# Performance work log

Hardware: AMD Instinct MI355X
Metric: run time of the kernel (lower is better)

## Reference

```python
import jax, jax.numpy as jnp
import numpy as np

B = 1; C = 96; NH = 4; HD = 24; WIN = 3; LL = 27; SR = 8
Dd, Hh, Ww = 16, 40, 40
N = Dd * Hh * Ww
pH, pW, pD = Hh // SR, Ww // SR, Dd // SR
PL = pH * pW * pD
T = 4096


def _build_mask():
    p = WIN // 2
    m = np.zeros((Dd + 2 * p, Hh + 2 * p, Ww + 2 * p), bool)
    m[p:Dd + p, p:Hh + p, p:Ww + p] = True
    pats = np.stack([m[dz:dz + Dd, dy:dy + Hh, dx:dx + Ww]
                     for dz in range(WIN) for dy in range(WIN) for dx in range(WIN)], axis=-1)
    return jnp.asarray(~pats.reshape(N, LL))  # True where padded (masked)

MASK = _build_mask()


def _layernorm(x, w, b, eps=1e-5):
    mu = jnp.mean(x, axis=-1, keepdims=True)
    var = jnp.var(x, axis=-1, keepdims=True)
    return (x - mu) / jnp.sqrt(var + eps) * w + b


def _l2(x, eps=1e-12):
    n = jnp.sqrt(jnp.sum(x * x, axis=-1, keepdims=True))
    return x / jnp.maximum(n, eps)


def _unfold3d(x):
    # x: (B,C,D,H,W) -> (B,C,N,27), kernel order (kd,kh,kw) as torch unfold(2).unfold(3).unfold(4)
    p = WIN // 2
    xp = jnp.pad(x, ((0, 0), (0, 0), (p, p), (p, p), (p, p)))
    pats = [xp[:, :, dz:dz + Dd, dy:dy + Hh, dx:dx + Ww]
            for dz in range(WIN) for dy in range(WIN) for dx in range(WIN)]
    return jnp.stack(pats, axis=-1).reshape(x.shape[0], C, N, LL)


def _conv3(x, w):
    return jax.lax.conv_general_dilated(x, w, (1, 1, 1), 'SAME',
                                        dimension_numbers=('NCDHW', 'OIDHW', 'NCDHW'))


def _bn(x, p, eps=1e-5):
    sh = (1, C, 1, 1, 1)
    return (x - p[2].reshape(sh)) / jnp.sqrt(p[3].reshape(sh) + eps) * p[0].reshape(sh) + p[1].reshape(sh)


def _lrelu(x):
    return jnp.where(x >= 0, x, 0.01 * x)


def _resblock(x, w1, p1, w2, p2):
    h = _lrelu(_bn(_conv3(x, w1), p1))
    h = _bn(_conv3(h, w2), p2)
    return _lrelu(h + x)


def _forward(x, relative_pos_index, relative_coords_table, seq_length_scale,
             norm_w, norm_b, gamma, w_qkvv, temperature, temperature2, query_embedding,
             rel_bias_local, learnable_tokens, learnable_bias, sr_w, sr_b,
             epa_norm_w, epa_norm_b, w_kv, cpb1_w, cpb1_b, cpb2_w, cpb2_b,
             out1_w, out1_b, out2_w, out2_b,
             c51a_w, c51a_bn, c51b_w, c51b_bn, c52a_w, c52a_bn, c52b_w, c52b_bn,
             conv8_w, conv8_b):
    Bq = x.shape[0]
    # flatten (D,H,W) -> N tokens; pos_embed=True adds 1.0 (faithful to `x + True`)
    xt = x.reshape(Bq, C, N).transpose(0, 2, 1) + 1.0
    xn = _layernorm(xt, norm_w, norm_b)
    qkvv = (xn @ w_qkvv.T).reshape(Bq, N, 4, NH, HD).transpose(2, 0, 3, 1, 4)
    q, k, v_ca, v_sa = qkvv[0], qkvv[1], qkvv[2], qkvv[3]  # (B,NH,N,HD)
    qn = _l2(q)
    qs = (qn + query_embedding) * (jax.nn.softplus(temperature) * seq_length_scale)
    k_img = k.transpose(0, 1, 3, 2).reshape(Bq, C, Dd, Hh, Ww)
    v_img = v_sa.transpose(0, 1, 3, 2).reshape(Bq, C, Dd, Hh, Ww)
    k_loc = _unfold3d(k_img).reshape(Bq, NH, HD, N, LL).transpose(0, 1, 3, 2, 4)  # (B,NH,N,HD,LL)
    v_loc = _unfold3d(v_img).reshape(Bq, NH, HD, N, LL).transpose(0, 1, 3, 2, 4)
    a_loc = jnp.einsum('bhnd,bhndk->bhnk', qs, k_loc) + rel_bias_local[:, None, :]
    a_loc = jnp.where(MASK[None, None], -jnp.inf, a_loc)
    # pooled branch (note faithful (H,W,D) reshape as in source)
    xp = xn.transpose(0, 2, 1).reshape(Bq, C, Hh, Ww, Dd)
    xp = jax.nn.gelu(jnp.einsum('oc,bcxyz->boxyz', sr_w, xp)
                     + sr_b[None, :, None, None, None], approximate=False)
    xp = xp.reshape(Bq, C, pH, SR, pW, SR, pD, SR).mean(axis=(3, 5, 7))  # adaptive avg pool
    xp = xp.reshape(Bq, C, PL).transpose(0, 2, 1)
    xp = _layernorm(xp, epa_norm_w, epa_norm_b)
    kv = (xp @ w_kv.T).reshape(Bq, PL, 2 * NH, HD).transpose(0, 2, 1, 3)
    k_pool, v_pool = kv[:, :NH], kv[:, NH:]
    tab = jax.nn.relu(relative_coords_table @ cpb1_w.T + cpb1_b) @ cpb2_w.T + cpb2_b  # (T,NH)
    pool_bias = jnp.take(tab.T, relative_pos_index.reshape(-1), axis=1).reshape(NH, N, PL)
    a_pool = jnp.einsum('bhnd,bhpd->bhnp', qs, _l2(k_pool)) + pool_bias[None]
    attn = jax.nn.softmax(jnp.concatenate([a_loc, a_pool], axis=-1), axis=-1)
    a_loc, a_pool = attn[..., :LL], attn[..., LL:]
    a_loc = jnp.einsum('bhnd,hdk->bhnk', qn, learnable_tokens) + learnable_bias[None] + a_loc
    x_loc = jnp.einsum('bhnk,bhndk->bhnd', a_loc, v_loc)
    x_pool = jnp.einsum('bhnp,bhpd->bhnd', a_pool, v_pool)
    x_sa = (x_loc + x_pool).transpose(0, 2, 1, 3).reshape(Bq, N, C)
    # channel attention branch
    qt = _l2(q.transpose(0, 1, 3, 2))
    kt = _l2(k.transpose(0, 1, 3, 2))
    vt = v_ca.transpose(0, 1, 3, 2)
    a_ca = jax.nn.softmax(jnp.einsum('bhdn,bhen->bhde', qt, kt) * temperature2, axis=-1)
    x_ca = jnp.einsum('bhde,bhen->bhdn', a_ca, vt).transpose(0, 3, 1, 2).reshape(Bq, N, C)
    epa = jnp.concatenate([x_sa @ out1_w.T + out1_b, x_ca @ out2_w.T + out2_b], axis=-1)
    ax = xt + gamma * epa
    skip = ax.reshape(Bq, Hh, Ww, Dd, C).transpose(0, 4, 1, 2, 3)  # (B,C,H,W,D)
    h = _resblock(skip, c51a_w, c51a_bn, c51b_w, c51b_bn)
    h = _resblock(h, c52a_w, c52a_bn, c52b_w, c52b_bn)
    return skip + jnp.einsum('oc,bcxyz->boxyz', conv8_w, h) + conv8_b[None, :, None, None, None]


def setup_inputs():
    key = jax.random.key(0)
    ks = iter(jax.random.split(key, 64))
    r = lambda shape, s=0.02: jax.random.normal(next(ks), shape, jnp.float32) * s
    d = {}
    d['x'] = jax.random.normal(next(ks), (B, C, Dd, Hh, Ww), jnp.float32)
    d['relative_pos_index'] = jax.random.randint(next(ks), (N * PL,), 0, T, jnp.int32)
    d['relative_coords_table'] = jax.random.normal(next(ks), (T, 3), jnp.float32)
    d['seq_length_scale'] = jnp.ones((1,), jnp.float32)
    d['norm_w'] = 1.0 + r((C,)); d['norm_b'] = r((C,))
    d['gamma'] = jnp.full((C,), 0.01, jnp.float32)
    d['w_qkvv'] = r((4 * C, C))
    d['temperature'] = jnp.full((NH, 1, 1), float(np.log(np.exp(1 / 0.24) - 1)), jnp.float32)
    d['temperature2'] = jnp.ones((NH, 1, 1), jnp.float32)
    d['query_embedding'] = r((NH, 1, HD))
    d['rel_bias_local'] = r((NH, LL), 0.0004)
    d['learnable_tokens'] = r((NH, HD, LL))
    d['learnable_bias'] = jnp.zeros((NH, 1, LL), jnp.float32)
    d['sr_w'] = r((C, C)); d['sr_b'] = r((C,))
    d['epa_norm_w'] = 1.0 + r((C,)); d['epa_norm_b'] = r((C,))
    d['w_kv'] = r((2 * C, C))
    d['cpb1_w'] = r((512, 3)); d['cpb1_b'] = r((512,))
    d['cpb2_w'] = r((NH, 512)); d['cpb2_b'] = r((NH,))
    d['out1_w'] = r((C // 2, C)); d['out1_b'] = r((C // 2,))
    d['out2_w'] = r((C // 2, C)); d['out2_b'] = r((C // 2,))
    bn = lambda: jnp.stack([1.0 + r((C,)), r((C,)), jnp.zeros((C,), jnp.float32), jnp.ones((C,), jnp.float32)])
    d['c51a_w'] = r((C, C, 3, 3, 3)); d['c51a_bn'] = bn()
    d['c51b_w'] = r((C, C, 3, 3, 3)); d['c51b_bn'] = bn()
    d['c52a_w'] = r((C, C, 3, 3, 3)); d['c52a_bn'] = bn()
    d['c52b_w'] = r((C, C, 3, 3, 3)); d['c52b_bn'] = bn()
    d['conv8_w'] = r((C, C)); d['conv8_b'] = r((C,))
    return d


def reference(x, relative_pos_index, relative_coords_table, seq_length_scale,
              norm_w, norm_b, gamma, w_qkvv, temperature, temperature2, query_embedding,
              rel_bias_local, learnable_tokens, learnable_bias, sr_w, sr_b,
              epa_norm_w, epa_norm_b, w_kv, cpb1_w, cpb1_b, cpb2_w, cpb2_b,
              out1_w, out1_b, out2_w, out2_b,
              c51a_w, c51a_bn, c51b_w, c51b_bn, c52a_w, c52a_bn, c52b_w, c52b_bn,
              conv8_w, conv8_b):
    return _forward(x, relative_pos_index, relative_coords_table, seq_length_scale,
                    norm_w, norm_b, gamma, w_qkvv, temperature, temperature2, query_embedding,
                    rel_bias_local, learnable_tokens, learnable_bias, sr_w, sr_b,
                    epa_norm_w, epa_norm_b, w_kv, cpb1_w, cpb1_b, cpb2_w, cpb2_b,
                    out1_w, out1_b, out2_w, out2_b,
                    c51a_w, c51a_bn, c51b_w, c51b_bn, c52a_w, c52a_bn, c52b_w, c52b_bn,
                    conv8_w, conv8_b)
```

## Files before the change

### kernel.cpp

```cpp
#include <hip/hip_runtime.h>
#include <hip/hip_bf16.h>

#define NN 25600
#define CC 96
#define NHh 4
#define HDd 24
#define SSLOT 2457600
#define WP 269568

typedef unsigned short ushort_t;
typedef float f32x4 __attribute__((ext_vector_type(4)));
typedef short s16x8 __attribute__((ext_vector_type(8)));
typedef _Float16 f16;
typedef f16 h2v __attribute__((ext_vector_type(2)));

__device__ __forceinline__ float LD(const void* p, int i){
  return ((const float*)p)[i];
}
__device__ __forceinline__ float b2f(ushort_t u){ return __uint_as_float(((unsigned)u)<<16); }
__device__ __forceinline__ ushort_t f2b(float f){
  unsigned u = __float_as_uint(f);
  unsigned r = (u + 0x7fffu + ((u>>16)&1u))>>16;
  return (ushort_t)r;
}
__device__ __forceinline__ ushort_t f2h(float f){
  f16 hv = (f16)f;
  return *reinterpret_cast<ushort_t*>(&hv);
}
__device__ __forceinline__ float fdot2(h2v a, h2v b, float c){
#if __has_builtin(__builtin_amdgcn_fdot2)
  return __builtin_amdgcn_fdot2(a, b, c, false);
#else
  return c + (float)a[0]*(float)b[0] + (float)a[1]*(float)b[1];
#endif
}
__device__ __forceinline__ void gl_lds16(const void* g, const void* l){
  __builtin_amdgcn_global_load_lds(
      (const __attribute__((address_space(1))) unsigned*)g,
      (__attribute__((address_space(3))) unsigned*)l, 16, 0, 0);
}

#define NEGINF (-3.0e38f)

__global__ __launch_bounds__(256) void k_mega(
    const void* w0, const void* w1, const void* w2, const void* w3,
    const void* wq, const void* wsr, const void* w8,
    const void* o1w, const void* o1b, const void* o2w, const void* o2b,
    const void* b0, const void* b1, const void* b2bn, const void* b3,
    const void* ltok,
    ushort_t* __restrict__ WB2, ushort_t* __restrict__ WQH,
    ushort_t* __restrict__ WSH, ushort_t* __restrict__ W8H,
    ushort_t* __restrict__ WE, float* __restrict__ EB,
    float* __restrict__ BNS, ushort_t* __restrict__ LTOKT,
    float* __restrict__ ZB,
    const int* __restrict__ rpi, int* __restrict__ rpiT,
    const void* __restrict__ x, const void* __restrict__ nw,
    const void* __restrict__ nb, ushort_t* __restrict__ XNH,
    const void* __restrict__ rct, const void* __restrict__ w1t,
    const void* __restrict__ b1t, const void* __restrict__ w2t,
    const void* __restrict__ b2t, float* __restrict__ TAB)
{
  __shared__ __align__(16) char SMEM[15400];
  int b = blockIdx.x, tid = threadIdx.x;
  if(b < 4212){
    int e = b*256 + tid;
    {
      int t = e/WP, r = e%WP;
      int tap = r/9984, r2 = r%9984, o = r2/104, p = r2%104;
      const void* w = (t==0)? w0 : (t==1)? w1 : (t==2)? w2 : w3;
      WB2[e] = (p<96)? f2b(LD(w, (o*96+p)*27 + tap)) : (ushort_t)0;
    }
    if(e < 36864) WQH[e] = f2b(LD(wq,e));
    if(e < 9216){ WSH[e] = f2b(LD(wsr,e)); W8H[e] = f2b(LD(w8,e)); }
    if(e < 96*192){
      int o = e/192, c2 = e%192;
      float v = 0.f;
      if(o < 48 && c2 < 96)        v = LD(o1w, o*96 + c2);
      else if(o >= 48 && c2 >= 96) v = LD(o2w, (o-48)*96 + (c2-96));
      WE[e] = f2b(v);
      if(c2 == 0) EB[o] = (o<48)? LD(o1b,o) : LD(o2b,o-48);
    }
    if(e < 384){
      int t = e/96, o = e%96;
      const void* bn = (t==0)? b0 : (t==1)? b1 : (t==2)? b2bn : b3;
      float g=LD(bn,o), bb=LD(bn,96+o), mu=LD(bn,192+o), var=LD(bn,288+o);
      float s = g*rsqrtf(var+1e-5f);
      BNS[t*192+o] = s;
      BNS[t*192+96+o] = bb - mu*s;
    }
    if(e < 4096){
      int h = e/1024, r = e%1024, kk = r/32, d = r%32;
      float v = (d<24 && kk<27)? LD(ltok, (h*24+d)*27 + kk) : 0.f;
      LTOKT[e] = f2b(v);
    }
    if(e < 8) ZB[e] = 0.f;
  } else if(b < 4612){
    int* T = (int*)SMEM;
    int n0 = (b-4212)*64;
    for(int f=tid; f<3200; f+=256){
      int nl = f/50, p = f%50;
      T[p*65+nl] = rpi[n0*50 + f];
    }
    __syncthreads();
    for(int f=tid; f<3200; f+=256){
      int p = f>>6, nl = f&63;
      rpiT[(size_t)p*NN + n0 + nl] = T[p*65+nl];
    }
  } else if(b < 5012){
    float* reds  = (float*)SMEM;
    float* redss = reds + 256;
    ushort_t* OUT = (ushort_t*)(redss + 256);
    int bx = b - 4612;
    int nl = tid&63, cg = tid>>6;
    int n = bx*64 + nl;
    float v[24]; float s=0.f, ss=0.f;
    #pragma unroll
    for(int i=0;i<24;i++){
      float t = LD(x, (cg*24+i)*NN + n) + 1.0f;
      v[i]=t; s+=t; ss+=t*t;
    }
    reds[cg*64+nl]=s; redss[cg*64+nl]=ss;
    __syncthreads();
    float S  = reds[nl]+reds[64+nl]+reds[128+nl]+reds[192+nl];
    float SS = redss[nl]+redss[64+nl]+redss[128+nl]+redss[192+nl];
    float mu = S*(1.0f/CC);
    float inv = rsqrtf(SS*(1.0f/CC) - mu*mu + 1e-5f);
    #pragma unroll
    for(int i=0;i<24;i++){
      int c = cg*24+i;
      OUT[nl*100+c] = f2b((v[i]-mu)*inv*LD(nw,c) + LD(nb,c));
    }
    __syncthreads();
    for(int f=tid; f<3072; f+=256){
      int r = f/48, dp = f%48;
      unsigned pk = (unsigned)OUT[r*100+dp*2] | ((unsigned)OUT[r*100+dp*2+1]<<16);
      *reinterpret_cast<unsigned*>(XNH + (size_t)(bx*64+r)*96 + dp*2) = pk;
    }
  } else {
    float* red = (float*)SMEM;
    int tt = b - 5012, j = tid;
    float r0=LD(rct,tt*3), r1=LD(rct,tt*3+1), r2=LD(rct,tt*3+2);
    float hA = r0*LD(w1t,j*3) + r1*LD(w1t,j*3+1) + r2*LD(w1t,j*3+2) + LD(b1t,j);
    hA = fmaxf(hA, 0.f);
    int j2 = j + 256;
    float hB = r0*LD(w1t,j2*3) + r1*LD(w1t,j2*3+1) + r2*LD(w1t,j2*3+2) + LD(b1t,j2);
    hB = fmaxf(hB, 0.f);
    int lane=j&63, wid=j>>6;
    for(int h=0;h<4;h++){
      float v = hA*LD(w2t, h*512+j) + hB*LD(w2t, h*512+j2);
      #pragma unroll
      for(int off=32;off;off>>=1) v += __shfl_down(v, off);
      if(lane==0) red[wid*4+h]=v;
    }
    __syncthreads();
    if(j<4){
      float s = red[j] + red[4+j] + red[8+j] + red[12+j];
      TAB[tt*4+j] = s + LD(b2t,j);
    }
  }
}

__global__ __launch_bounds__(256,2) void k_qkvsr(
    const ushort_t* __restrict__ XNH, const ushort_t* __restrict__ WQH,
    const ushort_t* __restrict__ WSH, const void* __restrict__ srb,
    float* __restrict__ out, ushort_t* __restrict__ KH,
    ushort_t* __restrict__ VH, float* __restrict__ XP2){
  int tid=threadIdx.x, w=tid>>6, lane=tid&63, lan=lane&15, grp=lane>>4;
  int n = blockIdx.x*64 + w*16 + lan;
  const ushort_t* bp = XNH + n*96;
  if(blockIdx.y < 2){
    int ybase = blockIdx.y*192;
    f32x4 acc[12];
    #pragma unroll
    for(int mt=0;mt<12;mt++) acc[mt] = (f32x4)(0.f);
    #pragma unroll
    for(int s=0;s<3;s++){
      s16x8 b = *reinterpret_cast<const s16x8*>(bp + s*32 + grp*8);
      #pragma unroll
      for(int mt=0;mt<12;mt++){
        s16x8 a = *reinterpret_cast<const s16x8*>(WQH + (ybase+mt*16+lan)*96 + s*32 + grp*8);
        acc[mt] = __builtin_amdgcn_mfma_f32_16x16x32_bf16(a, b, acc[mt], 0,0,0);
      }
    }
    #pragma unroll
    for(int mt=0;mt<12;mt++){
      int o0 = ybase + mt*16 + grp*4;
      int sl = o0/96, rr = o0%96, h = rr/24, dd = rr%24;
      f32x4 v = acc[mt];
      if(sl == 3){
        ushort4 pk = { f2h(v[0]), f2h(v[1]), f2h(v[2]), f2h(v[3]) };
        *reinterpret_cast<ushort4*>(VH + ((size_t)h*NN+n)*24 + dd) = pk;
      } else {
        *reinterpret_cast<float4*>(out + sl*SSLOT + ((size_t)h*NN+n)*24 + dd) =
            (float4){v[0],v[1],v[2],v[3]};
        if(sl == 1){
          ushort4 pk = { f2h(v[0]), f2h(v[1]), f2h(v[2]), f2h(v[3]) };
          *reinterpret_cast<ushort4*>(KH + ((size_t)h*NN+n)*24 + dd) = pk;
        }
      }
    }
  } else {
    f32x4 acc[6];
    #pragma unroll
    for(int mt=0;mt<6;mt++) acc[mt] = (f32x4)(0.f);
    #pragma unroll
    for(int s=0;s<3;s++){
      s16x8 b = *reinterpret_cast<const s16x8*>(bp + s*32 + grp*8);
      #pragma unroll
      for(int mt=0;mt<6;mt++){
        s16x8 a = *reinterpret_cast<const s16x8*>(WSH + (mt*16+lan)*96 + s*32 + grp*8);
        acc[mt] = __builtin_amdgcn_mfma_f32_16x16x32_bf16(a, b, acc[mt], 0,0,0);
      }
    }
    #pragma unroll
    for(int mt=0;mt<6;mt++){
      #pragma unroll
      for(int r=0;r<4;r++){
        int o = mt*16 + grp*4 + r;
        float y = acc[mt][r] + LD(srb,o);
        y = 0.5f*y*(1.0f + erff(y*0.70710678118f));
        XP2[o*NN+n] = y;
      }
    }
  }
}

__global__ __launch_bounds__(256) void k_mid1(
    const float* __restrict__ Q, const void* __restrict__ temp,
    const void* __restrict__ sls, const void* __restrict__ qe,
    const ushort_t* __restrict__ LTOKT, const void* __restrict__ lbias,
    float* __restrict__ QS, ushort_t* __restrict__ LTH,
    const float* __restrict__ XP2, float* __restrict__ pooled)
{
  __shared__ ushort_t QL[4][64][32];
  int b = blockIdx.x, tid = threadIdx.x;
  if(b < 400){
    int h = tid>>6, nl = tid&63;
    int n0 = b*64, n = n0 + nl;
    const float* qr = Q + ((size_t)h*NN+n)*24;
    float qv[24]; float ssum=0.f;
    #pragma unroll
    for(int d=0;d<24;d++){ qv[d]=qr[d]; ssum+=qv[d]*qv[d]; }
    float inv = 1.0f/fmaxf(sqrtf(ssum), 1e-12f);
    float t = LD(temp,h);
    float sp = log1pf(expf(t)) * LD(sls,0);
    float* qs = QS + ((size_t)h*NN+n)*24;
    #pragma unroll
    for(int d=0;d<24;d+=2){
      float q0 = qv[d]*inv, q1 = qv[d+1]*inv;
      unsigned pk = (unsigned)f2b(q0) | ((unsigned)f2b(q1)<<16);
      *reinterpret_cast<unsigned*>(&QL[h][nl][d]) = pk;
      qs[d]   = (q0 + LD(qe, h*24+d))*sp;
      qs[d+1] = (q1 + LD(qe, h*24+d+1))*sp;
    }
    *reinterpret_cast<unsigned*>(&QL[h][nl][24]) = 0;
    *reinterpret_cast<unsigned*>(&QL[h][nl][26]) = 0;
    *reinterpret_cast<unsigned*>(&QL[h][nl][28]) = 0;
    *reinterpret_cast<unsigned*>(&QL[h][nl][30]) = 0;
    __syncthreads();
    int lane=tid&63, lan=lane&15, grp=lane>>4;
    f32x4 acc[4][2];
    #pragma unroll
    for(int j=0;j<4;j++)
      #pragma unroll
      for(int tt=0;tt<2;tt++) acc[j][tt] = (f32x4)(0.f);
    #pragma unroll
    for(int j=0;j<4;j++){
      s16x8 bb = *reinterpret_cast<const s16x8*>(&QL[h][j*16+lan][grp*8]);
      #pragma unroll
      for(int tt=0;tt<2;tt++){
        s16x8 a = *reinterpret_cast<const s16x8*>(LTOKT + h*1024 + (tt*16+lan)*32 + grp*8);
        acc[j][tt] = __builtin_amdgcn_mfma_f32_16x16x32_bf16(a, bb, acc[j][tt], 0,0,0);
      }
    }
    #pragma unroll
    for(int j=0;j<4;j++){
      int nn = n0 + j*16 + lan;
      #pragma unroll
      for(int tt=0;tt<2;tt++){
        int k0 = tt*16 + grp*4;
        if(k0 < 28){
          ushort4 pk;
          ushort_t* pp = reinterpret_cast<ushort_t*>(&pk);
          #pragma unroll
          for(int r=0;r<4;r++){
            int k = k0+r;
            float v = acc[j][tt][r] + ((k<27)? LD(lbias, h*27+k) : 0.f);
            pp[r] = f2h(v);
          }
          *reinterpret_cast<ushort4*>(LTH + ((size_t)h*NN+nn)*28 + k0) = pk;
        }
      }
    }
  } else {
    int w = tid>>6, lane = tid&63;
    int pb = (b-400)*4 + w;
    int c = pb % CC, p = pb / CC;
    int ph = p/10, pw = (p%10)/2, pd = p%2;
    float s = 0.f;
    for(int t=lane; t<512; t+=64){
      int i=t>>6, j=(t>>3)&7, k=t&7;
      int m = (ph*8+i)*640 + (pw*8+j)*16 + (pd*8+k);
      s += XP2[c*NN+m];
    }
    #pragma unroll
    for(int off=32;off;off>>=1) s += __shfl_down(s, off);
    if(lane==0) pooled[p*CC+c] = s*(1.0f/512.0f);
  }
}

__global__ void k_mid2(const float* __restrict__ pooled, const void* __restrict__ ew,
                       const void* __restrict__ eb, const void* __restrict__ wkv,
                       ushort_t* __restrict__ KPNH, ushort_t* __restrict__ VPH){
  __shared__ float row[96], lnr[96], st[2], kk[96];
  int p = blockIdx.x, t = threadIdx.x;
  if(t<96) row[t] = pooled[p*96+t];
  __syncthreads();
  if(t==0){
    float s=0.f, ss=0.f;
    for(int c=0;c<96;c++){ float v=row[c]; s+=v; ss+=v*v; }
    float mu=s*(1.0f/96.0f);
    float var=ss*(1.0f/96.0f)-mu*mu;
    st[0]=mu; st[1]=rsqrtf(var+1e-5f);
  }
  __syncthreads();
  if(t<96) lnr[t] = (row[t]-st[0])*st[1]*LD(ew,t) + LD(eb,t);
  __syncthreads();
  if(t<192){
    float a=0.f;
    for(int c=0;c<96;c++) a += LD(wkv, t*96+c)*lnr[c];
    int g=t/24, d=t%24;
    if(g<4) kk[t]=a;
    else    VPH[((g-4)*50+p)*24+d] = f2h(a);
  }
  __syncthreads();
  if(t<96){
    int g=t/24, d=t%24;
    float ss=0.f;
    #pragma unroll
    for(int e=0;e<24;e++){ float v=kk[g*24+e]; ss+=v*v; }
    float inv = 1.0f/fmaxf(sqrtf(ss),1e-12f);
    KPNH[((g*50+p)*24)+d] = f2h(kk[t]*inv);
  }
}

__global__ __launch_bounds__(512) void k_big(
    const float* __restrict__ QS, const ushort_t* __restrict__ KH,
    const ushort_t* __restrict__ VH,
    const ushort_t* __restrict__ KPNH, const ushort_t* __restrict__ VPH,
    const float* __restrict__ TAB, const int* __restrict__ rpiT,
    const void* __restrict__ rbl, const ushort_t* __restrict__ LTH,
    ushort_t* __restrict__ XH,
    const float* __restrict__ Q, const float* __restrict__ K,
    float* __restrict__ PAR)
{
  __shared__ ushort_t KVH[2][600*26];
  int bb = blockIdx.x, tid = threadIdx.x;
  if(bb >= 64){
    int bb2 = bb - 64;
    int tile = bb2 % 100, h = bb2 / 100;
    int g = tile/25, sp = tile%25, hg = sp/5, wg = sp%5;
    int role = tid>>8, q = tid & 255;
    int wq = q>>6, l = q&63;
    int hy = l>>3, wx = l&7;
    int d0 = g*4 + wq;
    int h0 = hg*8+hy, w0 = wg*8+wx;
    int n = d0*1600 + h0*40 + w0;

    const ushort_t* KHh = KH + (size_t)h*NN*24;
    const ushort_t* VHh = VH + (size_t)h*NN*24;
    for(int f=tid; f<3600; f+=512){
      int t = f/1800, rem = f%1800, row = rem/3, qq = rem%3;
      int dr = row/100, yr = (row%100)/10, xr = row%10;
      int zc = min(max(g*4+dr-1,0),15), yc = min(max(hg*8+yr-1,0),39), xc = min(max(wg*8+xr-1,0),39);
      const ushort_t* src = (t? VHh : KHh) + (size_t)(zc*1600+yc*40+xc)*24 + qq*8;
      const unsigned* s32 = reinterpret_cast<const unsigned*>(src);
      unsigned a0=s32[0], a1=s32[1], a2=s32[2], a3=s32[3];
      unsigned* d32 = reinterpret_cast<unsigned*>(&KVH[t][row*26 + qq*8]);
      d32[0]=a0; d32[1]=a1; d32[2]=a2; d32[3]=a3;
    }

    h2v qp[12];
    {
      const float* qsp = QS + ((size_t)h*NN+n)*24;
      #pragma unroll
      for(int d=0; d<24; d+=4){
        float4 a = *reinterpret_cast<const float4*>(qsp+d);
        qp[d/2]   = (h2v){ (f16)a.x, (f16)a.y };
        qp[d/2+1] = (h2v){ (f16)a.z, (f16)a.w };
      }
    }
    __syncthreads();

    float m_r, s_r;
    h2v accA[12], accT[12];
    #pragma unroll
    for(int j=0;j<12;j++){ accA[j]=(h2v){(f16)0.f,(f16)0.f}; accT[j]=(h2v){(f16)0.f,(f16)0.f}; }

    const h2v* kph = reinterpret_cast<const h2v*>(KPNH) + (size_t)h*50*12;
    const h2v* vph = reinterpret_cast<const h2v*>(VPH)  + (size_t)h*50*12;

    if(role==0){
      float av[39]; unsigned okm=0;
      #pragma unroll
      for(int k=0;k<27;k++){
        int kz=k/9, ky=(k%9)/3, kx=k%3;
        bool ok = (unsigned)(d0+kz-1)<16u && (unsigned)(h0+ky-1)<40u && (unsigned)(w0+kx-1)<40u;
        float sc = NEGINF;
        if(ok){
          okm |= 1u<<k;
          const h2v* kr = reinterpret_cast<const h2v*>(
              &KVH[0][((wq+kz)*100 + (hy+ky)*10 + (wx+kx))*26]);
          sc = LD(rbl, h*27+k);
          #pragma unroll
          for(int j=0;j<12;j++) sc = fdot2(kr[j], qp[j], sc);
        }
        av[k]=sc;
      }
      #pragma unroll
      for(int p=0;p<12;p++){
        float sc = TAB[rpiT[(size_t)p*NN+n]*4 + h];
        const h2v* kr = kph + p*12;
        #pragma unroll
        for(int j=0;j<12;j++) sc = fdot2(kr[j], qp[j], sc);
        av[27+p]=sc;
      }
      float m = av[0];
      #pragma unroll
      for(int k=1;k<39;k++) m = fmaxf(m, av[k]);
      const f16* ltp = reinterpret_cast<const f16*>(LTH) + ((size_t)h*NN+n)*28;
      float s = 0.f;
      #pragma unroll
      for(int k=0;k<27;k++){
        if(okm>>k & 1u){
          int kz=k/9, ky=(k%9)/3, kx=k%3;
          float e = __expf(av[k]-m);
          s += e;
          float ltv = (float)ltp[k];
          h2v we = { (f16)e, (f16)e };
          h2v wt = { (f16)ltv, (f16)ltv };
          const h2v* vr = reinterpret_cast<const h2v*>(
              &KVH[1][((wq+kz)*100 + (hy+ky)*10 + (wx+kx))*26]);
          #pragma unroll
          for(int j=0;j<12;j++){
            accA[j] = vr[j]*we + accA[j];
            accT[j] = vr[j]*wt + accT[j];
          }
        }
      }
      #pragma unroll
      for(int p=0;p<12;p++){
        float e = __expf(av[27+p]-m);
        s += e;
        h2v we = { (f16)e, (f16)e };
        const h2v* vr = vph + p*12;
        #pragma unroll
        for(int j=0;j<12;j++) accA[j] = vr[j]*we + accA[j];
      }
      m_r = m; s_r = s;
    } else {
      float av[38];
      #pragma unroll
      for(int p=0;p<38;p++){
        int pp = p+12;
        float sc = TAB[rpiT[(size_t)pp*NN+n]*4 + h];
        const h2v* kr = kph + pp*12;
        #pragma unroll
        for(int j=0;j<12;j++) sc = fdot2(kr[j], qp[j], sc);
        av[p]=sc;
      }
      float m = av[0];
      #pragma unroll
      for(int p=1;p<38;p++) m = fmaxf(m, av[p]);
      float s = 0.f;
      #pragma unroll
      for(int p=0;p<38;p++){
        float e = __expf(av[p]-m);
        s += e;
        h2v we = { (f16)e, (f16)e };
        const h2v* vr = vph + (p+12)*12;
        #pragma unroll
        for(int j=0;j<12;j++) accA[j] = vr[j]*we + accA[j];
      }
      m_r = m; s_r = s;
    }
    __syncthreads();

    float* PP = (float*)&KVH[0][0];
    if(role==1){
      PP[q*15+0] = m_r;
      PP[q*15+1] = s_r;
      #pragma unroll
      for(int j=0;j<12;j++){
        h2v a = accA[j];
        PP[q*15+2+j] = __uint_as_float(*reinterpret_cast<unsigned*>(&a));
      }
    }
    __syncthreads();

    float* TRF = (float*)&KVH[0][0] + 4096;
    if(role==0){
      float mp = PP[q*15+0], sp2 = PP[q*15+1];
      float m = fmaxf(m_r, mp);
      float a = __expf(m_r - m), b = __expf(mp - m);
      float inv = 1.0f/(a*s_r + b*sp2);
      #pragma unroll
      for(int j=0;j<12;j++){
        unsigned pb = __float_as_uint(PP[q*15+2+j]);
        h2v ap = *reinterpret_cast<h2v*>(&pb);
        float v0 = (a*(float)accA[j][0] + b*(float)ap[0])*inv + (float)accT[j][0];
        float v1 = (a*(float)accA[j][1] + b*(float)ap[1])*inv + (float)accT[j][1];
        TRF[q*25 + 2*j]   = v0;
        TRF[q*25 + 2*j+1] = v1;
      }
    }
    __syncthreads();

    for(int f=tid; f<3072; f+=512){
      int q2 = f/12, dp = f%12;
      int w2 = q2>>6, l2 = q2&63;
      int n2 = (g*4+w2)*1600 + (hg*8+(l2>>3))*40 + (wg*8+(l2&7));
      float v0 = TRF[q2*25+dp*2], v1 = TRF[q2*25+dp*2+1];
      unsigned pk = (unsigned)f2b(v0) | ((unsigned)f2b(v1)<<16);
      *reinterpret_cast<unsigned*>(XH + (size_t)n2*192 + h*24 + dp*2) = pk;
    }
  } else {
    float* WRED = (float*)&KVH[0][0];
    int b2 = bb;
    int h = b2 >> 4, chunk = b2 & 15;
    int wv = tid >> 6, lane = tid & 63;
    int n0 = chunk*1600 + wv*200;
    const float* Qh = Q + (size_t)h*NN*24;
    const float* Kh = K + (size_t)h*NN*24;
    int r = lane/6, cgl = lane%6;
    bool act = lane < 36;
    int d1 = r*4, d2 = cgl*4;
    float accm[4][4];
    #pragma unroll
    for(int i=0;i<4;i++)
      #pragma unroll
      for(int j=0;j<4;j++) accm[i][j]=0.f;
    float qss4[4] = {0.f,0.f,0.f,0.f}, kss4[4] = {0.f,0.f,0.f,0.f};
    if(act){
      #pragma unroll 4
      for(int i=0;i<200;i++){
        int n = n0 + i;
        float4 q4 = *reinterpret_cast<const float4*>(Qh + (size_t)n*24 + d1);
        float4 k4 = *reinterpret_cast<const float4*>(Kh + (size_t)n*24 + d2);
        float qa[4] = {q4.x,q4.y,q4.z,q4.w};
        float ka[4] = {k4.x,k4.y,k4.z,k4.w};
        #pragma unroll
        for(int i2=0;i2<4;i2++)
          #pragma unroll
          for(int j=0;j<4;j++) accm[i2][j] += qa[i2]*ka[j];
        #pragma unroll
        for(int e=0;e<4;e++){ qss4[e]+=qa[e]*qa[e]; kss4[e]+=ka[e]*ka[e]; }
      }
      float* wp = WRED + (wv*36 + lane)*25;
      #pragma unroll
      for(int i=0;i<4;i++)
        #pragma unroll
        for(int j=0;j<4;j++) wp[i*4+j] = accm[i][j];
      if(r == cgl){
        #pragma unroll
        for(int e=0;e<4;e++){ wp[16+e]=qss4[e]; wp[20+e]=kss4[e]; }
      }
    }
    __syncthreads();
    for(int c=tid; c<624; c+=512){
      float s = 0.f;
      if(c < 576){
        int d1o = c/24, d2o = c%24;
        int li = (d1o>>2)*6 + (d2o>>2);
        int sl = (d1o&3)*4 + (d2o&3);
        #pragma unroll
        for(int w8=0;w8<8;w8++) s += WRED[(w8*36+li)*25+sl];
        PAR[((size_t)chunk*96 + h*24 + d1o)*26 + d2o] = s;
      } else {
        int cc = c - 576;
        int d = cc % 24, isk = cc / 24;
        int li = (d>>2)*7;
        int sl = 16 + isk*4 + (d&3);
        #pragma unroll
        for(int w8=0;w8<8;w8++) s += WRED[(w8*36+li)*25+sl];
        PAR[((size_t)chunk*96 + h*24 + d)*26 + 24 + isk] = s;
      }
    }
  }
}

__global__ __launch_bounds__(256) void k_caep(
    const float* __restrict__ PAR, const void* __restrict__ t2,
    const float* __restrict__ VCA, ushort_t* __restrict__ XH){
  __shared__ float A[2304];
  __shared__ float kinv_s[96];
  int t = threadIdx.x;
  float S[24]; float qi=0.f;
  int hh = (t<96)? t/24 : 0;
  if(t<96){
    float qss=0.f, kss=0.f;
    #pragma unroll
    for(int e=0;e<24;e++) S[e]=0.f;
    for(int c=0;c<16;c++){
      const float* pp = PAR + ((size_t)c*96+t)*26;
      #pragma unroll
      for(int e=0;e<24;e++) S[e] += pp[e];
      qss += pp[24]; kss += pp[25];
    }
    qi = 1.0f/fmaxf(sqrtf(qss),1e-12f);
    kinv_s[t] = 1.0f/fmaxf(sqrtf(kss),1e-12f);
  }
  __syncthreads();
  if(t<96){
    float tv = LD(t2,hh);
    float v[24]; float m = NEGINF;
    #pragma unroll
    for(int e=0;e<24;e++){
      v[e] = S[e]*qi*kinv_s[hh*24+e]*tv;
      m = fmaxf(m, v[e]);
    }
    float s=0.f;
    #pragma unroll
    for(int e=0;e<24;e++){ v[e]=__expf(v[e]-m); s+=v[e]; }
    float inv=1.0f/s;
    #pragma unroll
    for(int e=0;e<24;e++) A[t*24+e] = v[e]*inv;
  }
  __syncthreads();
  int h = t>>6, l = t&63;
  int n = blockIdx.x*64 + l;
  float vr[24];
  const float* vp = VCA + ((size_t)h*NN+n)*24;
  #pragma unroll
  for(int e=0;e<24;e+=4){
    float4 v = *reinterpret_cast<const float4*>(vp+e);
    vr[e]=v.x; vr[e+1]=v.y; vr[e+2]=v.z; vr[e+3]=v.w;
  }
  float o[24];
  #pragma unroll
  for(int d=0;d<24;d++){
    float a=0.f;
    const float* ar = A + (h*24+d)*24;
    #pragma unroll
    for(int e=0;e<24;e++) a += ar[e]*vr[e];
    o[d]=a;
  }
  #pragma unroll
  for(int d=0;d<24;d+=2){
    unsigned pk = (unsigned)f2b(o[d]) | ((unsigned)f2b(o[d+1])<<16);
    *reinterpret_cast<unsigned*>(XH + (size_t)n*192 + 96 + h*24 + d) = pk;
  }
}

__global__ __launch_bounds__(256,2) void k_epam(
    const ushort_t* __restrict__ XH, const ushort_t* __restrict__ WE,
    const float* __restrict__ EB, const void* __restrict__ x,
    const void* __restrict__ gamma,
    float* __restrict__ SKIPF, ushort_t* __restrict__ SKIPH){
  int tid=threadIdx.x, w=tid>>6, lane=tid&63, lan=lane&15, grp=lane>>4;
  int n = blockIdx.x*64 + w*16 + lan;
  const ushort_t* bp = XH + (size_t)n*192;
  f32x4 acc[6];
  #pragma unroll
  for(int mt=0;mt<6;mt++) acc[mt] = (f32x4)(0.f);
  #pragma unroll
  for(int s=0;s<6;s++){
    s16x8 b = *reinterpret_cast<const s16x8*>(bp + s*32 + grp*8);
    #pragma unroll
    for(int mt=0;mt<6;mt++){
      s16x8 a = *reinterpret_cast<const s16x8*>(WE + (mt*16+lan)*192 + s*32 + grp*8);
      acc[mt] = __builtin_amdgcn_mfma_f32_16x16x32_bf16(a, b, acc[mt], 0,0,0);
    }
  }
  #pragma unroll
  for(int mt=0;mt<6;mt++){
    #pragma unroll
    for(int r=0;r<4;r++){
      int o = mt*16 + grp*4 + r;
      float e = acc[mt][r] + EB[o];
      float v = LD(x, o*NN+n) + 1.0f + LD(gamma,o)*e;
      SKIPF[(size_t)n*96+o] = v;
      SKIPH[(size_t)n*96+o] = f2b(v);
    }
  }
}

__global__ __launch_bounds__(256,2) void k_convm8(
    const ushort_t* __restrict__ IN, const ushort_t* __restrict__ WB2,
    const float* __restrict__ BNS, const float* __restrict__ resf,
    const float* __restrict__ ZB,
    ushort_t* __restrict__ outh, float* __restrict__ outf)
{
  __shared__ ushort_t BUF[2][16640];
  int tid = threadIdx.x;
  int w = tid>>6, lane = tid&63;
  int lan = lane&15, grp = lane>>4;
  int bs = (blockIdx.x&7)*50 + (blockIdx.x>>3);
  int n0 = bs*64;

  auto STAGE = [&](int tap, ushort_t* buf){
    int dx=tap/9-1, dy=(tap%9)/3-1, dz=tap%3-1;
    int off = dx*640 + dy*16 + dz;
    const ushort_t* wsrc = WB2 + tap*9984;
    #pragma unroll
    for(int i=0;i<9;i++){
      int cb = i*256 + w*64;
      if(cb >= 2080) break;
      int c = cb + lane;
      const void* src;
      if(c < 1248){
        src = wsrc + c*8;
      } else {
        int c2 = c - 1248;
        int r = c2/13, p = c2%13;
        int nn = n0 + r;
        int X = nn/640, rr2 = nn%640, Y = rr2/16, Z = nn&15;
        bool ok = (p<12) && (unsigned)(X+dx)<40u && (unsigned)(Y+dy)<40u && (unsigned)(Z+dz)<16u;
        src = ok ? (const void*)(IN + (size_t)(nn+off)*96 + p*8) : (const void*)ZB;
      }
      if(c < 2080) gl_lds16(src, buf + cb*8);
    }
  };

  f32x4 acc[6];
  #pragma unroll
  for(int mt=0;mt<6;mt++) acc[mt] = (f32x4)(0.f);

  STAGE(0, BUF[0]);
  asm volatile("s_waitcnt vmcnt(0)" ::: "memory");
  __builtin_amdgcn_s_barrier();

  for(int tap=0; tap<27; ++tap){
    if(tap<26){
      STAGE(tap+1, BUF[(tap+1)&1]);
      asm volatile("s_waitcnt vmcnt(8)" ::: "memory");
    } else {
      asm volatile("s_waitcnt vmcnt(0)" ::: "memory");
    }
    __builtin_amdgcn_s_barrier();
    __builtin_amdgcn_sched_barrier(0);
    const ushort_t* Ab = BUF[tap&1];
    const ushort_t* Bb = Ab + 9984;
    s16x8 bfr[3];
    #pragma unroll
    for(int s=0;s<3;s++)
      bfr[s] = *reinterpret_cast<const s16x8*>(Bb + (w*16+lan)*104 + s*32 + grp*8);
    #pragma unroll
    for(int mt=0;mt<6;mt++){
      #pragma unroll
      for(int s=0;s<3;s++){
        s16x8 a = *reinterpret_cast<const s16x8*>(Ab + (mt*16+lan)*104 + s*32 + grp*8);
        acc[mt] = __builtin_amdgcn_mfma_f32_16x16x32_bf16(a, bfr[s], acc[mt], 0,0,0);
      }
    }
    __builtin_amdgcn_s_barrier();
  }

  float* TR = (float*)&BUF[0][0];
  int nl = w*16 + lan;
  #pragma unroll
  for(int mt=0;mt<6;mt++){
    int ob = mt*16 + grp*4;
    float4 vv;
    vv.x = acc[mt][0]*BNS[ob+0] + BNS[96+ob+0];
    vv.y = acc[mt][1]*BNS[ob+1] + BNS[96+ob+1];
    vv.z = acc[mt][2]*BNS[ob+2] + BNS[96+ob+2];
    vv.w = acc[mt][3]*BNS[ob+3] + BNS[96+ob+3];
    *reinterpret_cast<float4*>(TR + nl*100 + ob) = vv;
  }
  __syncthreads();
  for(int f=tid; f<3072; f+=256){
    int r = f/48, cp = f%48;
    int n = n0 + r;
    float v0 = TR[r*100+cp*2], v1 = TR[r*100+cp*2+1];
    if(resf){ v0 += resf[(size_t)n*96+cp*2]; v1 += resf[(size_t)n*96+cp*2+1]; }
    v0 = (v0>=0.f)? v0 : 0.01f*v0;
    v1 = (v1>=0.f)? v1 : 0.01f*v1;
    unsigned pk = (unsigned)f2b(v0) | ((unsigned)f2b(v1)<<16);
    *reinterpret_cast<unsigned*>(outh + (size_t)n*96 + cp*2) = pk;
    if(outf){
      float2 fo; fo.x=v0; fo.y=v1;
      *reinterpret_cast<float2*>(outf + (size_t)n*96 + cp*2) = fo;
    }
  }
}

__global__ __launch_bounds__(256,2) void k_finm(
    const float* __restrict__ SKIPF, const ushort_t* __restrict__ T3H,
    const ushort_t* __restrict__ W8H, const void* __restrict__ b,
    float* __restrict__ out){
  int tid=threadIdx.x, w=tid>>6, lane=tid&63, lan=lane&15, grp=lane>>4;
  int n = blockIdx.x*64 + w*16 + lan;
  const ushort_t* bp = T3H + n*96;
  f32x4 acc[6];
  #pragma unroll
  for(int mt=0;mt<6;mt++) acc[mt] = (f32x4)(0.f);
  #pragma unroll
  for(int s=0;s<3;s++){
    s16x8 bb = *reinterpret_cast<const s16x8*>(bp + s*32 + grp*8);
    #pragma unroll
    for(int mt=0;mt<6;mt++){
      s16x8 a = *reinterpret_cast<const s16x8*>(W8H + (mt*16+lan)*96 + s*32 + grp*8);
      acc[mt] = __builtin_amdgcn_mfma_f32_16x16x32_bf16(a, bb, acc[mt], 0,0,0);
    }
  }
  #pragma unroll
  for(int mt=0;mt<6;mt++){
    #pragma unroll
    for(int r=0;r<4;r++){
      int o = mt*16 + grp*4 + r;
      out[o*NN+n] = SKIPF[(size_t)n*96+o] + acc[mt][r] + LD(b,o);
    }
  }
}

extern "C" void kernel_launch(void* const* d_in, const int* in_sizes, int n_in,
                              void* d_out, int out_size, void* d_ws, size_t ws_size,
                              hipStream_t stream){
  const void* x     = d_in[0];
  const int*  rpi   = (const int*)d_in[1];
  const void* rct   = d_in[2];
  const void* sls   = d_in[3];
  const void* nw    = d_in[4];
  const void* nb    = d_in[5];
  const void* gamma = d_in[6];
  const void* wqkvv = d_in[7];
  const void* temp  = d_in[8];
  const void* temp2 = d_in[9];
  const void* qe    = d_in[10];
  const void* rbl   = d_in[11];
  const void* ltok  = d_in[12];
  const void* lbias = d_in[13];
  const void* srw   = d_in[14];
  const void* srb   = d_in[15];
  const void* epaw  = d_in[16];
  const void* epab  = d_in[17];
  const void* wkv   = d_in[18];
  const void* c1w   = d_in[19];
  const void* c1b   = d_in[20];
  const void* c2w   = d_in[21];
  const void* c2b   = d_in[22];
  const void* o1w   = d_in[23];
  const void* o1b   = d_in[24];
  const void* o2w   = d_in[25];
  const void* o2b   = d_in[26];
  const void* w51a  = d_in[27];
  const void* bn51a = d_in[28];
  const void* w51b  = d_in[29];
  const void* bn51b = d_in[30];
  const void* w52a  = d_in[31];
  const void* bn52a = d_in[32];
  const void* w52b  = d_in[33];
  const void* bn52b = d_in[34];
  const void* w8    = d_in[35];
  const void* b8    = d_in[36];

  float* ws = (float*)d_ws;
  const size_t S = SSLOT;
  ushort_t* XNH = (ushort_t*)ws;
  float* SKIPF = ws;
  float* Q     = ws + 1*S;
  float* Kb    = ws + 2*S;
  float* T2F   = ws + 2*S;
  float* VCA   = ws + 3*S;
  ushort_t* KH = (ushort_t*)(ws + 4*S);
  ushort_t* VH = KH + SSLOT;
  float* QS    = ws + 6*S;
  ushort_t* XH = (ushort_t*)(ws + 7*S);
  int*   rpiT  = (int*)(ws + 8*S);
  float* XP2   = ws + 7*S;
  ushort_t* SKIPH = (ushort_t*)(ws + 4*S);
  ushort_t* T1H   = SKIPH + SSLOT;
  ushort_t* T2H   = (ushort_t*)(ws + 5*S);
  ushort_t* T3H   = T2H + SSLOT;
  float* SM  = ws + 9*S;
  float* pooled = SM;
  float* TAB    = SM + 19200;
  ushort_t* WB2 = (ushort_t*)(SM + 40960);
  float* BNS    = SM + 40960 + 539136;
  ushort_t* WQH = (ushort_t*)(BNS + 768);
  ushort_t* WSH = WQH + 36864;
  ushort_t* W8H = WSH + 9216;
  ushort_t* WE  = W8H + 9216;
  float* EB     = BNS + 768 + 18432 + 4608 + 4608 + 9216;
  float* PAR    = EB + 96;
  ushort_t* KPNH = (ushort_t*)(PAR + 39936);
  ushort_t* VPH  = KPNH + 4800;
  ushort_t* LTOKT= VPH + 4800;
  ushort_t* LTH  = LTOKT + 4096;
  float* ZB      = (float*)(LTH + 2867200);

  k_mega  <<<9108, 256, 0, stream>>>(w51a, w51b, w52a, w52b, wqkvv, srw, w8,
                                     o1w, o1b, o2w, o2b,
                                     bn51a, bn51b, bn52a, bn52b, ltok,
                                     WB2, WQH, WSH, W8H, WE, EB, BNS, LTOKT, ZB,
                                     rpi, rpiT,
                                     x, nw, nb, XNH,
                                     rct, c1w, c1b, c2w, c2b, TAB);
  k_qkvsr <<<dim3(400,3), 256, 0, stream>>>(XNH, WQH, WSH, srb, Q, KH, VH, XP2);
  k_mid1  <<<1600, 256, 0, stream>>>(Q, temp, sls, qe, LTOKT, lbias, QS, LTH,
                                     XP2, pooled);
  k_mid2  <<<50,   256, 0, stream>>>(pooled, epaw, epab, wkv, KPNH, VPH);
  k_big   <<<464,  512, 0, stream>>>(QS, KH, VH, KPNH, VPH, TAB, rpiT,
                                     rbl, LTH, XH, Q, Kb, PAR);
  k_caep  <<<400,  256, 0, stream>>>(PAR, temp2, VCA, XH);
  k_epam  <<<400,  256, 0, stream>>>(XH, WE, EB, x, gamma, SKIPF, SKIPH);
  k_convm8<<<400, 256, 0, stream>>>(SKIPH, WB2,        BNS,     nullptr, ZB, T1H, nullptr);
  k_convm8<<<400, 256, 0, stream>>>(T1H,   WB2+WP,     BNS+192, SKIPF,   ZB, T2H, T2F);
  k_convm8<<<400, 256, 0, stream>>>(T2H,   WB2+2*WP,   BNS+384, nullptr, ZB, T1H, nullptr);
  k_convm8<<<400, 256, 0, stream>>>(T1H,   WB2+3*WP,   BNS+576, T2F,     ZB, T3H, nullptr);
  k_finm  <<<400, 256, 0, stream>>>(SKIPF, T3H, W8H, b8, (float*)d_out);
}
```

Measured before the change: 275.8 us.

## Fuse channel-attention into EPA projection and final 1x1 conv into last conv

Merges k_caep and k_epam into one kernel that stages each 64-token row block of XH in shared memory, writes the channel-attention output there, and runs the projection MFMA straight from LDS. It also folds k_finm into the last k_convm8 launch: the conv result goes to LDS and is multiplied by the conv8 weights in place. This drops two launches and the global round trips through XH's second half and T3H. In exchange it adds 25.6KB of shared memory to the fused kernel, which can lower occupancy.

```diff
diff --git a/kernel.cpp b/kernel.cpp
--- a/kernel.cpp
+++ b/kernel.cpp
@@ -589,12 +589,18 @@
   }
 }
 
-__global__ __launch_bounds__(256) void k_caep(
+__global__ __launch_bounds__(256) void k_caepam(
     const float* __restrict__ PAR, const void* __restrict__ t2,
-    const float* __restrict__ VCA, ushort_t* __restrict__ XH){
+    const float* __restrict__ VCA, const ushort_t* __restrict__ XH,
+    const ushort_t* __restrict__ WE, const float* __restrict__ EB,
+    const void* __restrict__ x, const void* __restrict__ gamma,
+    float* __restrict__ SKIPF, ushort_t* __restrict__ SKIPH)
+{
   __shared__ float A[2304];
   __shared__ float kinv_s[96];
+  __shared__ ushort_t XR[64*200];
   int t = threadIdx.x;
+  int n0 = blockIdx.x*64;
   float S[24]; float qi=0.f;
   int hh = (t<96)? t/24 : 0;
   if(t<96){
@@ -627,39 +633,36 @@
     for(int e=0;e<24;e++) A[t*24+e] = v[e]*inv;
   }
   __syncthreads();
-  int h = t>>6, l = t&63;
-  int n = blockIdx.x*64 + l;
-  float vr[24];
-  const float* vp = VCA + ((size_t)h*NN+n)*24;
-  #pragma unroll
-  for(int e=0;e<24;e+=4){
-    float4 v = *reinterpret_cast<const float4*>(vp+e);
-    vr[e]=v.x; vr[e+1]=v.y; vr[e+2]=v.z; vr[e+3]=v.w;
-  }
-  float o[24];
-  #pragma unroll
-  for(int d=0;d<24;d++){
-    float a=0.f;
-    const float* ar = A + (h*24+d)*24;
-    #pragma unroll
-    for(int e=0;e<24;e++) a += ar[e]*vr[e];
-    o[d]=a;
-  }
-  #pragma unroll
-  for(int d=0;d<24;d+=2){
-    unsigned pk = (unsigned)f2b(o[d]) | ((unsigned)f2b(o[d+1])<<16);
-    *reinterpret_cast<unsigned*>(XH + (size_t)n*192 + 96 + h*24 + d) = pk;
-  }
-}
-
-__global__ __launch_bounds__(256,2) void k_epam(
-    const ushort_t* __restrict__ XH, const ushort_t* __restrict__ WE,
-    const float* __restrict__ EB, const void* __restrict__ x,
-    const void* __restrict__ gamma,
-    float* __restrict__ SKIPF, ushort_t* __restrict__ SKIPH){
-  int tid=threadIdx.x, w=tid>>6, lane=tid&63, lan=lane&15, grp=lane>>4;
-  int n = blockIdx.x*64 + w*16 + lan;
-  const ushort_t* bp = XH + (size_t)n*192;
+  for(int f=t; f<3072; f+=256){
+    int r = f/48, dp = f%48;
+    unsigned pk = *reinterpret_cast<const unsigned*>(XH + (size_t)(n0+r)*192 + dp*2);
+    *reinterpret_cast<unsigned*>(&XR[r*200 + dp*2]) = pk;
+  }
+  {
+    int h = t>>6, l = t&63;
+    int n = n0 + l;
+    float vr[24];
+    const float* vp = VCA + ((size_t)h*NN+n)*24;
+    #pragma unroll
+    for(int e=0;e<24;e+=4){
+      float4 v = *reinterpret_cast<const float4*>(vp+e);
+      vr[e]=v.x; vr[e+1]=v.y; vr[e+2]=v.z; vr[e+3]=v.w;
+    }
+    #pragma unroll
+    for(int d=0;d<24;d+=2){
+      float a0=0.f, a1=0.f;
+      const float* ar0 = A + (h*24+d)*24;
+      const float* ar1 = ar0 + 24;
+      #pragma unroll
+      for(int e=0;e<24;e++){ a0 += ar0[e]*vr[e]; a1 += ar1[e]*vr[e]; }
+      unsigned pk = (unsigned)f2b(a0) | ((unsigned)f2b(a1)<<16);
+      *reinterpret_cast<unsigned*>(&XR[l*200 + 96 + h*24 + d]) = pk;
+    }
+  }
+  __syncthreads();
+  int w=t>>6, lane=t&63, lan=lane&15, grp=lane>>4;
+  int n = n0 + w*16 + lan;
+  const ushort_t* bp = &XR[(w*16+lan)*200];
   f32x4 acc[6];
   #pragma unroll
   for(int mt=0;mt<6;mt++) acc[mt] = (f32x4)(0.f);
@@ -689,7 +692,9 @@
     const ushort_t* __restrict__ IN, const ushort_t* __restrict__ WB2,
     const float* __restrict__ BNS, const float* __restrict__ resf,
     const float* __restrict__ ZB,
-    ushort_t* __restrict__ outh, float* __restrict__ outf)
+    ushort_t* __restrict__ outh, float* __restrict__ outf,
+    const ushort_t* __restrict__ W8H8, const void* __restrict__ fb8,
+    const float* __restrict__ skipf, float* __restrict__ finout)
 {
   __shared__ ushort_t BUF[2][16640];
   int tid = threadIdx.x;
@@ -757,6 +762,7 @@
   }
 
   float* TR = (float*)&BUF[0][0];
+  ushort_t* FR = &BUF[1][0];
   int nl = w*16 + lan;
   #pragma unroll
   for(int mt=0;mt<6;mt++){
@@ -777,39 +783,39 @@
     v0 = (v0>=0.f)? v0 : 0.01f*v0;
     v1 = (v1>=0.f)? v1 : 0.01f*v1;
     unsigned pk = (unsigned)f2b(v0) | ((unsigned)f2b(v1)<<16);
-    *reinterpret_cast<unsigned*>(outh + (size_t)n*96 + cp*2) = pk;
-    if(outf){
-      float2 fo; fo.x=v0; fo.y=v1;
-      *reinterpret_cast<float2*>(outf + (size_t)n*96 + cp*2) = fo;
-    }
-  }
-}
-
-__global__ __launch_bounds__(256,2) void k_finm(
-    const float* __restrict__ SKIPF, const ushort_t* __restrict__ T3H,
-    const ushort_t* __restrict__ W8H, const void* __restrict__ b,
-    float* __restrict__ out){
-  int tid=threadIdx.x, w=tid>>6, lane=tid&63, lan=lane&15, grp=lane>>4;
-  int n = blockIdx.x*64 + w*16 + lan;
-  const ushort_t* bp = T3H + n*96;
-  f32x4 acc[6];
-  #pragma unroll
-  for(int mt=0;mt<6;mt++) acc[mt] = (f32x4)(0.f);
-  #pragma unroll
-  for(int s=0;s<3;s++){
-    s16x8 bb = *reinterpret_cast<const s16x8*>(bp + s*32 + grp*8);
+    if(finout){
+      *reinterpret_cast<unsigned*>(&FR[r*104 + cp*2]) = pk;
+    } else {
+      *reinterpret_cast<unsigned*>(outh + (size_t)n*96 + cp*2) = pk;
+      if(outf){
+        float2 fo; fo.x=v0; fo.y=v1;
+        *reinterpret_cast<float2*>(outf + (size_t)n*96 + cp*2) = fo;
+      }
+    }
+  }
+  if(finout){
+    __syncthreads();
+    f32x4 acc2[6];
+    #pragma unroll
+    for(int mt=0;mt<6;mt++) acc2[mt] = (f32x4)(0.f);
+    const ushort_t* bp = &FR[(w*16+lan)*104];
+    #pragma unroll
+    for(int s=0;s<3;s++){
+      s16x8 bb = *reinterpret_cast<const s16x8*>(bp + s*32 + grp*8);
+      #pragma unroll
+      for(int mt=0;mt<6;mt++){
+        s16x8 a = *reinterpret_cast<const s16x8*>(W8H8 + (mt*16+lan)*96 + s*32 + grp*8);
+        acc2[mt] = __builtin_amdgcn_mfma_f32_16x16x32_bf16(a, bb, acc2[mt], 0,0,0);
+      }
+    }
+    int n = n0 + w*16 + lan;
     #pragma unroll
     for(int mt=0;mt<6;mt++){
-      s16x8 a = *reinterpret_cast<const s16x8*>(W8H + (mt*16+lan)*96 + s*32 + grp*8);
-      acc[mt] = __builtin_amdgcn_mfma_f32_16x16x32_bf16(a, bb, acc[mt], 0,0,0);
-    }
-  }
-  #pragma unroll
-  for(int mt=0;mt<6;mt++){
-    #pragma unroll
-    for(int r=0;r<4;r++){
-      int o = mt*16 + grp*4 + r;
-      out[o*NN+n] = SKIPF[(size_t)n*96+o] + acc[mt][r] + LD(b,o);
+      #pragma unroll
+      for(int r=0;r<4;r++){
+        int o = mt*16 + grp*4 + r;
+        finout[(size_t)o*NN+n] = skipf[(size_t)n*96+o] + acc2[mt][r] + LD(fb8,o);
+      }
     }
   }
 }
@@ -872,7 +878,6 @@
   ushort_t* SKIPH = (ushort_t*)(ws + 4*S);
   ushort_t* T1H   = SKIPH + SSLOT;
   ushort_t* T2H   = (ushort_t*)(ws + 5*S);
-  ushort_t* T3H   = T2H + SSLOT;
   float* SM  = ws + 9*S;
   float* pooled = SM;
   float* TAB    = SM + 19200;
@@ -903,11 +908,14 @@
   k_mid2  <<<50,   256, 0, stream>>>(pooled, epaw, epab, wkv, KPNH, VPH);
   k_big   <<<464,  512, 0, stream>>>(QS, KH, VH, KPNH, VPH, TAB, rpiT,
                                      rbl, LTH, XH, Q, Kb, PAR);
-  k_caep  <<<400,  256, 0, stream>>>(PAR, temp2, VCA, XH);
-  k_epam  <<<400,  256, 0, stream>>>(XH, WE, EB, x, gamma, SKIPF, SKIPH);
-  k_convm8<<<400, 256, 0, stream>>>(SKIPH, WB2,        BNS,     nullptr, ZB, T1H, nullptr);
-  k_convm8<<<400, 256, 0, stream>>>(T1H,   WB2+WP,     BNS+192, SKIPF,   ZB, T2H, T2F);
-  k_convm8<<<400, 256, 0, stream>>>(T2H,   WB2+2*WP,   BNS+384, nullptr, ZB, T1H, nullptr);
-  k_convm8<<<400, 256, 0, stream>>>(T1H,   WB2+3*WP,   BNS+576, T2F,     ZB, T3H, nullptr);
-  k_finm  <<<400, 256, 0, stream>>>(SKIPF, T3H, W8H, b8, (float*)d_out);
-}
+  k_caepam<<<400,  256, 0, stream>>>(PAR, temp2, VCA, XH, WE, EB, x, gamma,
+                                     SKIPF, SKIPH);
+  k_convm8<<<400, 256, 0, stream>>>(SKIPH, WB2,      BNS,     nullptr, ZB, T1H, nullptr,
+                                    nullptr, nullptr, nullptr, nullptr);
+  k_convm8<<<400, 256, 0, stream>>>(T1H,   WB2+WP,   BNS+192, SKIPF,   ZB, T2H, T2F,
+                                    nullptr, nullptr, nullptr, nullptr);
+  k_convm8<<<400, 256, 0, stream>>>(T2H,   WB2+2*WP, BNS+384, nullptr, ZB, T1H, nullptr,
+                                    nullptr, nullptr, nullptr, nullptr);
+  k_convm8<<<400, 256, 0, stream>>>(T1H,   WB2+3*WP, BNS+576, T2F,     ZB, nullptr, nullptr,
+                                    W8H, b8, SKIPF, (float*)d_out);
+}
```

Result: no change. 278.2 us (+0.9%).
